# Performance work log

Measured on AMD Instinct MI355X. Metric: run time of the kernel, lower is better.

The kernel has to match this reference:

```python
import jax, jax.numpy as jnp
import numpy as np

M = 50000   # query points
N = 50000   # support points (non-strided: M == N)
C = 128     # channels
H = 32      # neighborhood size
G = 8       # groups
CPG = C // G  # channels per group = 16
R = 1       # alpha_reduction
EPS = 1e-5
NEG_SLOPE = 0.1


def setup_inputs() -> dict:
    key = jax.random.key(0)
    ks = jax.random.split(key, 6)
    q_pts = jax.random.normal(ks[0], (M, 3), jnp.float32)
    s_pts = jax.random.normal(ks[1], (N, 3), jnp.float32)
    s_feats = jax.random.normal(ks[2], (N, C), jnp.float32)
    neighb_inds = jax.random.randint(ks[3], (M, H), 0, N)
    # alpha MLP params: UnaryBlock(C -> C//R) [Linear + BN + LeakyReLU], then Linear(C//R -> H*CPG)
    w1 = jax.random.normal(ks[4], (C, C // R), jnp.float32) * (1.0 / np.sqrt(C))
    b1 = jnp.zeros((C // R,), jnp.float32)
    gamma1 = jnp.ones((C // R,), jnp.float32)
    beta1 = jnp.zeros((C // R,), jnp.float32)
    w2 = jax.random.normal(ks[5], (C // R, H * CPG), jnp.float32) * (1.0 / np.sqrt(C // R))
    b2 = jnp.zeros((H * CPG,), jnp.float32)
    return {"q_pts": q_pts, "s_pts": s_pts, "s_feats": s_feats,
            "neighb_inds": neighb_inds,
            "w1": w1, "b1": b1, "gamma1": gamma1, "beta1": beta1,
            "w2": w2, "b2": b2}


def _alpha_mlp(x, w1, b1, gamma1, beta1, w2, b2):
    # UnaryBlock: Linear -> BatchNorm (training mode over point dim) -> LeakyReLU(0.1)
    h = x @ w1 + b1
    mu = jnp.mean(h, axis=0)
    var = jnp.var(h, axis=0)
    h = (h - mu) * jax.lax.rsqrt(var + EPS) * gamma1 + beta1
    h = jnp.where(h >= 0, h, NEG_SLOPE * h)
    return h @ w2 + b2  # (M, H*CPG)


def reference(q_pts, s_pts, s_feats, neighb_inds, w1, b1, gamma1, beta1, w2, b2):
    # pad support features with a zero "shadow" row so index N maps to zeros
    padded = jnp.concatenate([s_feats, jnp.zeros_like(s_feats[:1])], axis=0)  # (N+1, C)
    neighbor_feats = padded[neighb_inds]  # (M, H, C) gather
    # q_pts.shape[0] == s_pts.shape[0] -> non-strided: pooled feats are the support feats
    pooled_feats = s_feats  # (M, C)
    attn = _alpha_mlp(pooled_feats, w1, b1, gamma1, beta1, w2, b2)  # (M, H*CPG)
    # view: channels dim C splits row-major into (CPG, G)
    nb = neighbor_feats.reshape(M, H, CPG, G)
    a = attn.reshape(M, H, CPG)
    out = jnp.einsum('mhcg,mhc->mcg', nb, a)  # weighted neighbor reduction over H
    return out.reshape(M, C)
```

## Files before the change

### kernel.cpp

```cpp
#include <hip/hip_runtime.h>
#include <hip/hip_bf16.h>

#define MPTS  50000
#define NCH   128
#define NH    32
#define NK2   512
#define NEG   0.1f
#define BN_EPS 1e-5f
#define K1_BLOCKS 1563
#define TPAD_ROWS 50048
#define R1_CHUNK  17
#define R1_BLOCKS 92

typedef __attribute__((ext_vector_type(8))) short        short8;
typedef __attribute__((ext_vector_type(4))) float        float4v;
typedef __attribute__((ext_vector_type(2))) unsigned int uint2v;

__device__ __forceinline__ short f2b(float f) {
    __hip_bfloat16 h = __float2bfloat16(f);
    return *reinterpret_cast<short*>(&h);
}
__device__ __forceinline__ float b2f(short s) {
    unsigned int u = ((unsigned int)(unsigned short)s) << 16;
    return *reinterpret_cast<float*>(&u);
}

__global__ __launch_bounds__(64)
void k0_pack_w1(const float* __restrict__ w1, short* __restrict__ w1f) {
    int o = blockIdx.x * 64 + threadIdx.x;
    int i = o & 7, l = (o >> 3) & 63, ks = (o >> 9) & 3, nt = o >> 11;
    w1f[o] = f2b(w1[(ks * 32 + (l >> 4) * 8 + i) * NCH + nt * 16 + (l & 15)]);
}
__global__ __launch_bounds__(64)
void k0_pack_w2(const float* __restrict__ w2, short* __restrict__ w2f) {
    int o = blockIdx.x * 64 + threadIdx.x;
    int i = o & 7, l = (o >> 3) & 63, ks = (o >> 9) & 3, nt = o >> 11;
    w2f[o] = f2b(w2[(ks * 32 + (l >> 4) * 8 + i) * NK2 + nt * 16 + (l & 15)]);
}

__global__ __launch_bounds__(64)
void k1_gemm(const float* __restrict__ sf, const short* __restrict__ w1f,
             short* __restrict__ t, short* __restrict__ sfb,
             float* __restrict__ pS, float* __restrict__ pSS) {
    const int l = threadIdx.x, lr = l & 15, lg = l >> 4;
    const int m0 = blockIdx.x * 32;

    short8 af[2][4];
    #pragma unroll
    for (int mt = 0; mt < 2; ++mt) {
        const int row = m0 + mt * 16 + lr;
        const bool valid = row < MPTS;
        #pragma unroll
        for (int ks = 0; ks < 4; ++ks) {
            const int col = ks * 32 + lg * 8;
            float4v v0 = {0.f, 0.f, 0.f, 0.f}, v1 = {0.f, 0.f, 0.f, 0.f};
            if (valid) {
                const float4v* p = (const float4v*)(sf + (size_t)row * NCH + col);
                v0 = p[0]; v1 = p[1];
            }
            short8 av;
            av[0] = f2b(v0[0]); av[1] = f2b(v0[1]); av[2] = f2b(v0[2]); av[3] = f2b(v0[3]);
            av[4] = f2b(v1[0]); av[5] = f2b(v1[1]); av[6] = f2b(v1[2]); av[7] = f2b(v1[3]);
            af[mt][ks] = av;
            if (valid) *(short8*)(sfb + (size_t)row * NCH + col) = av;
        }
    }

    float4v acc[2][8];
    #pragma unroll
    for (int mt = 0; mt < 2; ++mt)
        #pragma unroll
        for (int nt = 0; nt < 8; ++nt) acc[mt][nt] = (float4v){0.f, 0.f, 0.f, 0.f};

    #pragma unroll
    for (int nt = 0; nt < 8; ++nt) {
        short8 bq[4];
        #pragma unroll
        for (int ks = 0; ks < 4; ++ks)
            bq[ks] = *(const short8*)(w1f + ((nt * 4 + ks) * 64 + l) * 8);
        #pragma unroll
        for (int ks = 0; ks < 4; ++ks) {
            acc[0][nt] = __builtin_amdgcn_mfma_f32_16x16x32_bf16(af[0][ks], bq[ks], acc[0][nt], 0, 0, 0);
            acc[1][nt] = __builtin_amdgcn_mfma_f32_16x16x32_bf16(af[1][ks], bq[ks], acc[1][nt], 0, 0, 0);
        }
    }

    #pragma unroll
    for (int nt = 0; nt < 8; ++nt) {
        const int cch = nt * 16 + lr;
        float s = 0.f, ss = 0.f;
        #pragma unroll
        for (int mt = 0; mt < 2; ++mt) {
            #pragma unroll
            for (int r = 0; r < 4; ++r) {
                const float v = acc[mt][nt][r];
                const int row = m0 + mt * 16 + lg * 4 + r;
                t[(size_t)row * NCH + cch] = f2b(v);
                s += v; ss += v * v;
            }
        }
        s  += __shfl_xor(s, 16);  s  += __shfl_xor(s, 32);
        ss += __shfl_xor(ss, 16); ss += __shfl_xor(ss, 32);
        if (lg == 0) {
            pS [blockIdx.x * NCH + cch] = s;
            pSS[blockIdx.x * NCH + cch] = ss;
        }
    }
}

__global__ __launch_bounds__(256)
void k2a_reduce(const float* __restrict__ pS, const float* __restrict__ pSS,
                float* __restrict__ qS, float* __restrict__ qSS) {
    const int c = threadIdx.x & 127, a = threadIdx.x >> 7;
    const float* __restrict__ src = a ? pSS : pS;
    const int b0 = blockIdx.x * R1_CHUNK;
    float s = 0.f;
    #pragma unroll
    for (int i = 0; i < R1_CHUNK; ++i) {
        const int b = b0 + i;
        if (b < K1_BLOCKS) s += src[b * NCH + c];
    }
    (a ? qSS : qS)[blockIdx.x * NCH + c] = s;
}

__global__ __launch_bounds__(256)
void k2b_coef(const float* __restrict__ qS, const float* __restrict__ qSS,
              const float* __restrict__ gamma, const float* __restrict__ beta,
              float* __restrict__ coef) {
    __shared__ float sh[256];
    const int c = threadIdx.x & 127, a = threadIdx.x >> 7;
    const float* __restrict__ src = a ? qSS : qS;
    float s0 = 0.f, s1 = 0.f, s2 = 0.f, s3 = 0.f;
    #pragma unroll
    for (int b = 0; b < R1_BLOCKS; b += 4) {
        s0 += src[(b + 0) * NCH + c];
        s1 += src[(b + 1) * NCH + c];
        s2 += src[(b + 2) * NCH + c];
        s3 += src[(b + 3) * NCH + c];
    }
    sh[threadIdx.x] = (s0 + s1) + (s2 + s3);
    __syncthreads();
    if (a == 0) {
        const float inv = 1.0f / (float)MPTS;
        const float mu  = sh[c] * inv;
        const float var = sh[128 + c] * inv - mu * mu;
        const float aa  = gamma[c] * rsqrtf(var + BN_EPS);
        coef[c]       = aa;
        coef[NCH + c] = beta[c] - mu * aa;
    }
}

__global__ __launch_bounds__(256)
void k3_fused(const short* __restrict__ t, const float* __restrict__ coef,
              const short* __restrict__ w2f, const float* __restrict__ b2,
              const short* __restrict__ sfb, const int* __restrict__ nidx,
              float* __restrict__ out) {
    __shared__ short hsh[512 * 8];
    __shared__ short attnT[NK2 * 36];
    __shared__ int   idxs[32 * NH];

    const int tid = threadIdx.x;
    const int m0  = blockIdx.x * 32;

    #pragma unroll
    for (int g = tid; g < 512; g += 256) {
        const int row = g >> 4, ch = g & 15;
        short8 tv = *(const short8*)(t + (size_t)(m0 + row) * NCH + ch * 8);
        const float4v* ca = (const float4v*)(coef + ch * 8);
        const float4v* cb = (const float4v*)(coef + NCH + ch * 8);
        const float4v a0 = ca[0], a1 = ca[1], b0 = cb[0], b1 = cb[1];
        short8 hv;
        #pragma unroll
        for (int j = 0; j < 4; ++j) {
            float x = b2f(tv[j]) * a0[j] + b0[j];
            x = (x >= 0.f) ? x : NEG * x;
            hv[j] = f2b(x);
        }
        #pragma unroll
        for (int j = 0; j < 4; ++j) {
            float x = b2f(tv[4 + j]) * a1[j] + b1[j];
            x = (x >= 0.f) ? x : NEG * x;
            hv[4 + j] = f2b(x);
        }
        *(short8*)&hsh[(row * 16 + (ch ^ (row & 15))) * 8] = hv;
    }
    for (int i2 = tid; i2 < 32 * NH; i2 += 256) {
        const int gi = m0 * NH + i2;
        idxs[i2] = (gi < MPTS * NH) ? nidx[gi] : 0;
    }
    __syncthreads();

    {
        const int l = tid & 63, w = tid >> 6, lr = l & 15, lg = l >> 4;
        short8 af[2][4];
        #pragma unroll
        for (int mt = 0; mt < 2; ++mt)
            #pragma unroll
            for (int ks = 0; ks < 4; ++ks)
                af[mt][ks] = *(const short8*)&hsh[((mt * 16 + lr) * 16 + ((ks * 4 + lg) ^ lr)) * 8];

        #pragma unroll
        for (int nti = 0; nti < 8; ++nti) {
            const int nt = w * 8 + nti;
            float4v acc0 = {0.f, 0.f, 0.f, 0.f}, acc1 = {0.f, 0.f, 0.f, 0.f};
            #pragma unroll
            for (int ks = 0; ks < 4; ++ks) {
                const short8 bq = *(const short8*)(w2f + ((nt * 4 + ks) * 64 + l) * 8);
                acc0 = __builtin_amdgcn_mfma_f32_16x16x32_bf16(af[0][ks], bq, acc0, 0, 0, 0);
                acc1 = __builtin_amdgcn_mfma_f32_16x16x32_bf16(af[1][ks], bq, acc1, 0, 0, 0);
            }
            const int   n    = nt * 16 + lr;
            const float bias = b2[n];
            {
                unsigned u0 = ((unsigned)(unsigned short)f2b(acc0[1] + bias) << 16) |
                               (unsigned short)f2b(acc0[0] + bias);
                unsigned u1 = ((unsigned)(unsigned short)f2b(acc0[3] + bias) << 16) |
                               (unsigned short)f2b(acc0[2] + bias);
                *(uint2v*)&attnT[n * 36 + 0 * 16 + lg * 4] = (uint2v){u0, u1};
            }
            {
                unsigned u0 = ((unsigned)(unsigned short)f2b(acc1[1] + bias) << 16) |
                               (unsigned short)f2b(acc1[0] + bias);
                unsigned u1 = ((unsigned)(unsigned short)f2b(acc1[3] + bias) << 16) |
                               (unsigned short)f2b(acc1[2] + bias);
                *(uint2v*)&attnT[n * 36 + 1 * 16 + lg * 4] = (uint2v){u0, u1};
            }
        }
    }
    __syncthreads();

    {
        const int q = tid & 31, pg = tid >> 5;
        const int c0 = q * 4, cpg = q >> 1;
        #pragma unroll
        for (int pi = 0; pi < 4; ++pi) {
            const int p = pg * 4 + pi, m = m0 + p;
            if (m >= MPTS) continue;
            float4v acc = {0.f, 0.f, 0.f, 0.f};
            #pragma unroll 16
            for (int h = 0; h < NH; ++h) {
                const int n = idxs[p * NH + h];
                const uint2v ld = *(const uint2v*)(sfb + (size_t)n * NCH + c0);
                const float wgt = b2f(attnT[(h * 16 + cpg) * 36 + p]);
                const short* fs = (const short*)&ld;
                acc[0] += b2f(fs[0]) * wgt;
                acc[1] += b2f(fs[1]) * wgt;
                acc[2] += b2f(fs[2]) * wgt;
                acc[3] += b2f(fs[3]) * wgt;
            }
            *(float4v*)(out + (size_t)m * NCH + c0) = acc;
        }
    }
}

extern "C" void kernel_launch(void* const* d_in, const int* in_sizes, int n_in,
                              void* d_out, int out_size, void* d_ws, size_t ws_size,
                              hipStream_t stream) {
    const float* sf    = (const float*)d_in[2];
    const int*   nidx  = (const int*)  d_in[3];
    const float* w1    = (const float*)d_in[4];
    const float* gamma = (const float*)d_in[6];
    const float* beta  = (const float*)d_in[7];
    const float* w2    = (const float*)d_in[8];
    const float* b2    = (const float*)d_in[9];
    float* out = (float*)d_out;

    short* t   = (short*)d_ws;
    short* sfb = t + (size_t)TPAD_ROWS * NCH;
    short* w1f = sfb + (size_t)TPAD_ROWS * NCH;
    short* w2f = w1f + 16384;
    float* pS  = (float*)(w2f + 65536);
    float* pSS = pS + (size_t)K1_BLOCKS * NCH;
    float* qS  = pSS + (size_t)K1_BLOCKS * NCH;
    float* qSS = qS + (size_t)R1_BLOCKS * NCH;
    float* coef = qSS + (size_t)R1_BLOCKS * NCH;

    k0_pack_w1<<<256,  64, 0, stream>>>(w1, w1f);
    k0_pack_w2<<<1024, 64, 0, stream>>>(w2, w2f);
    k1_gemm<<<K1_BLOCKS, 64, 0, stream>>>(sf, w1f, t, sfb, pS, pSS);
    k2a_reduce<<<R1_BLOCKS, 256, 0, stream>>>(pS, pSS, qS, qSS);
    k2b_coef<<<1, 256, 0, stream>>>(qS, qSS, gamma, beta, coef);
    k3_fused<<<K1_BLOCKS, 256, 0, stream>>>(t, coef, w2f, b2, sfb, nidx, out);
}
```

Before: 89.92 us.

## Store GEMM1 output in MFMA fragment layout, halve k3 tile, widen gather loads

k1 now writes the first GEMM result in MFMA accumulator-fragment order as packed 8-byte stores, instead of scattered 2-byte row-major stores. k3 reads those fragments directly for the BN/LeakyReLU prologue. k3 tiles are now 16 points per block, giving twice as many blocks and smaller LDS. The gather stage loads 16 bytes per lane (8 bf16 channels) instead of 8. The two weight-pack kernels are merged into one launch, and k1 runs four waves per block with padded tiles so k2a can drop its bounds checks. The aim is to cut scattered global writes, launch overhead and load instruction count, at the cost of fewer MFMA per block and reliance on padded workspace sizes (k1 tiles past MPTS must produce zero contributions).

```diff
diff --git a/kernel.cpp b/kernel.cpp
--- a/kernel.cpp
+++ b/kernel.cpp
@@ -7,14 +7,17 @@
 #define NK2   512
 #define NEG   0.1f
 #define BN_EPS 1e-5f
-#define K1_BLOCKS 1563
+#define K1T   1564
 #define TPAD_ROWS 50048
 #define R1_CHUNK  17
 #define R1_BLOCKS 92
+#define K3_BLOCKS 3125
+#define ATP 20
 
 typedef __attribute__((ext_vector_type(8))) short        short8;
 typedef __attribute__((ext_vector_type(4))) float        float4v;
 typedef __attribute__((ext_vector_type(2))) unsigned int uint2v;
+typedef __attribute__((ext_vector_type(4))) unsigned int uint4v;
 
 __device__ __forceinline__ short f2b(float f) {
     __hip_bfloat16 h = __float2bfloat16(f);
@@ -24,26 +27,36 @@
     unsigned int u = ((unsigned int)(unsigned short)s) << 16;
     return *reinterpret_cast<float*>(&u);
 }
+__device__ __forceinline__ float b2f_hi(unsigned int w) {
+    unsigned int u = w & 0xffff0000u;
+    return *reinterpret_cast<float*>(&u);
+}
+__device__ __forceinline__ float b2f_lo(unsigned int w) {
+    unsigned int u = w << 16;
+    return *reinterpret_cast<float*>(&u);
+}
 
 __global__ __launch_bounds__(64)
-void k0_pack_w1(const float* __restrict__ w1, short* __restrict__ w1f) {
-    int o = blockIdx.x * 64 + threadIdx.x;
-    int i = o & 7, l = (o >> 3) & 63, ks = (o >> 9) & 3, nt = o >> 11;
-    w1f[o] = f2b(w1[(ks * 32 + (l >> 4) * 8 + i) * NCH + nt * 16 + (l & 15)]);
-}
-__global__ __launch_bounds__(64)
-void k0_pack_w2(const float* __restrict__ w2, short* __restrict__ w2f) {
-    int o = blockIdx.x * 64 + threadIdx.x;
-    int i = o & 7, l = (o >> 3) & 63, ks = (o >> 9) & 3, nt = o >> 11;
-    w2f[o] = f2b(w2[(ks * 32 + (l >> 4) * 8 + i) * NK2 + nt * 16 + (l & 15)]);
-}
-
-__global__ __launch_bounds__(64)
+void k0_pack(const float* __restrict__ w1, const float* __restrict__ w2,
+             short* __restrict__ w1f, short* __restrict__ w2f) {
+    if (blockIdx.x < 256) {
+        int o = blockIdx.x * 64 + threadIdx.x;
+        int i = o & 7, l = (o >> 3) & 63, ks = (o >> 9) & 3, nt = o >> 11;
+        w1f[o] = f2b(w1[(ks * 32 + (l >> 4) * 8 + i) * NCH + nt * 16 + (l & 15)]);
+    } else {
+        int o = (blockIdx.x - 256) * 64 + threadIdx.x;
+        int i = o & 7, l = (o >> 3) & 63, ks = (o >> 9) & 3, nt = o >> 11;
+        w2f[o] = f2b(w2[(ks * 32 + (l >> 4) * 8 + i) * NK2 + nt * 16 + (l & 15)]);
+    }
+}
+
+__global__ __launch_bounds__(256)
 void k1_gemm(const float* __restrict__ sf, const short* __restrict__ w1f,
-             short* __restrict__ t, short* __restrict__ sfb,
+             uint2v* __restrict__ tfrag, short* __restrict__ sfb,
              float* __restrict__ pS, float* __restrict__ pSS) {
-    const int l = threadIdx.x, lr = l & 15, lg = l >> 4;
-    const int m0 = blockIdx.x * 32;
+    const int l = threadIdx.x & 63, lr = l & 15, lg = l >> 4;
+    const int tile = blockIdx.x * 4 + (threadIdx.x >> 6);
+    const int m0 = tile * 32;
 
     short8 af[2][4];
     #pragma unroll
@@ -91,19 +104,18 @@
         float s = 0.f, ss = 0.f;
         #pragma unroll
         for (int mt = 0; mt < 2; ++mt) {
-            #pragma unroll
-            for (int r = 0; r < 4; ++r) {
-                const float v = acc[mt][nt][r];
-                const int row = m0 + mt * 16 + lg * 4 + r;
-                t[(size_t)row * NCH + cch] = f2b(v);
-                s += v; ss += v * v;
-            }
+            const float4v a = acc[mt][nt];
+            unsigned u0 = ((unsigned)(unsigned short)f2b(a[1]) << 16) | (unsigned short)f2b(a[0]);
+            unsigned u1 = ((unsigned)(unsigned short)f2b(a[3]) << 16) | (unsigned short)f2b(a[2]);
+            tfrag[(size_t)((tile * 2 + mt) * 8 + nt) * 64 + l] = (uint2v){u0, u1};
+            s  += a[0] + a[1] + a[2] + a[3];
+            ss += a[0]*a[0] + a[1]*a[1] + a[2]*a[2] + a[3]*a[3];
         }
         s  += __shfl_xor(s, 16);  s  += __shfl_xor(s, 32);
         ss += __shfl_xor(ss, 16); ss += __shfl_xor(ss, 32);
         if (lg == 0) {
-            pS [blockIdx.x * NCH + cch] = s;
-            pSS[blockIdx.x * NCH + cch] = ss;
+            pS [tile * NCH + cch] = s;
+            pSS[tile * NCH + cch] = ss;
         }
     }
 }
@@ -116,10 +128,8 @@
     const int b0 = blockIdx.x * R1_CHUNK;
     float s = 0.f;
     #pragma unroll
-    for (int i = 0; i < R1_CHUNK; ++i) {
-        const int b = b0 + i;
-        if (b < K1_BLOCKS) s += src[b * NCH + c];
-    }
+    for (int i = 0; i < R1_CHUNK; ++i)
+        s += src[(b0 + i) * NCH + c];
     (a ? qSS : qS)[blockIdx.x * NCH + c] = s;
 }
 
@@ -151,105 +161,94 @@
 }
 
 __global__ __launch_bounds__(256)
-void k3_fused(const short* __restrict__ t, const float* __restrict__ coef,
+void k3_fused(const uint2v* __restrict__ tfrag, const float* __restrict__ coef,
               const short* __restrict__ w2f, const float* __restrict__ b2,
               const short* __restrict__ sfb, const int* __restrict__ nidx,
               float* __restrict__ out) {
-    __shared__ short hsh[512 * 8];
-    __shared__ short attnT[NK2 * 36];
-    __shared__ int   idxs[32 * NH];
+    __shared__ short hsh[16 * 128];
+    __shared__ short attnT[NK2 * ATP];
+    __shared__ int   idxs[16 * NH];
 
     const int tid = threadIdx.x;
-    const int m0  = blockIdx.x * 32;
-
-    #pragma unroll
-    for (int g = tid; g < 512; g += 256) {
-        const int row = g >> 4, ch = g & 15;
-        short8 tv = *(const short8*)(t + (size_t)(m0 + row) * NCH + ch * 8);
-        const float4v* ca = (const float4v*)(coef + ch * 8);
-        const float4v* cb = (const float4v*)(coef + NCH + ch * 8);
-        const float4v a0 = ca[0], a1 = ca[1], b0 = cb[0], b1 = cb[1];
-        short8 hv;
-        #pragma unroll
-        for (int j = 0; j < 4; ++j) {
-            float x = b2f(tv[j]) * a0[j] + b0[j];
-            x = (x >= 0.f) ? x : NEG * x;
-            hv[j] = f2b(x);
-        }
-        #pragma unroll
-        for (int j = 0; j < 4; ++j) {
-            float x = b2f(tv[4 + j]) * a1[j] + b1[j];
-            x = (x >= 0.f) ? x : NEG * x;
-            hv[4 + j] = f2b(x);
-        }
-        *(short8*)&hsh[(row * 16 + (ch ^ (row & 15))) * 8] = hv;
-    }
-    for (int i2 = tid; i2 < 32 * NH; i2 += 256) {
-        const int gi = m0 * NH + i2;
-        idxs[i2] = (gi < MPTS * NH) ? nidx[gi] : 0;
+    const int m0  = blockIdx.x * 16;
+
+    {
+        const int l = tid & 63, half = tid >> 6;
+        #pragma unroll
+        for (int k = 0; k < 2; ++k) {
+            const int nt = half + k * 4;
+            const uint2v v = tfrag[(size_t)blockIdx.x * 512 + nt * 64 + l];
+            const int col = nt * 16 + (l & 15);
+            const int rg  = (l >> 4) * 4;
+            const float a = coef[col];
+            const float b = coef[NCH + col];
+            const int ch  = col >> 3;
+            const int cb  = col & 7;
+            float x0 = b2f_lo(v[0]) * a + b;  x0 = (x0 >= 0.f) ? x0 : NEG * x0;
+            float x1 = b2f_hi(v[0]) * a + b;  x1 = (x1 >= 0.f) ? x1 : NEG * x1;
+            float x2 = b2f_lo(v[1]) * a + b;  x2 = (x2 >= 0.f) ? x2 : NEG * x2;
+            float x3 = b2f_hi(v[1]) * a + b;  x3 = (x3 >= 0.f) ? x3 : NEG * x3;
+            hsh[((rg + 0) * 16 + (ch ^ (rg + 0))) * 8 + cb] = f2b(x0);
+            hsh[((rg + 1) * 16 + (ch ^ (rg + 1))) * 8 + cb] = f2b(x1);
+            hsh[((rg + 2) * 16 + (ch ^ (rg + 2))) * 8 + cb] = f2b(x2);
+            hsh[((rg + 3) * 16 + (ch ^ (rg + 3))) * 8 + cb] = f2b(x3);
+        }
+        idxs[tid]       = nidx[(size_t)m0 * NH + tid];
+        idxs[tid + 256] = nidx[(size_t)m0 * NH + tid + 256];
     }
     __syncthreads();
 
     {
         const int l = tid & 63, w = tid >> 6, lr = l & 15, lg = l >> 4;
-        short8 af[2][4];
-        #pragma unroll
-        for (int mt = 0; mt < 2; ++mt)
-            #pragma unroll
-            for (int ks = 0; ks < 4; ++ks)
-                af[mt][ks] = *(const short8*)&hsh[((mt * 16 + lr) * 16 + ((ks * 4 + lg) ^ lr)) * 8];
+        short8 af[4];
+        #pragma unroll
+        for (int ks = 0; ks < 4; ++ks)
+            af[ks] = *(const short8*)&hsh[(lr * 16 + ((ks * 4 + lg) ^ lr)) * 8];
 
         #pragma unroll
         for (int nti = 0; nti < 8; ++nti) {
             const int nt = w * 8 + nti;
-            float4v acc0 = {0.f, 0.f, 0.f, 0.f}, acc1 = {0.f, 0.f, 0.f, 0.f};
+            float4v acc = {0.f, 0.f, 0.f, 0.f};
             #pragma unroll
             for (int ks = 0; ks < 4; ++ks) {
                 const short8 bq = *(const short8*)(w2f + ((nt * 4 + ks) * 64 + l) * 8);
-                acc0 = __builtin_amdgcn_mfma_f32_16x16x32_bf16(af[0][ks], bq, acc0, 0, 0, 0);
-                acc1 = __builtin_amdgcn_mfma_f32_16x16x32_bf16(af[1][ks], bq, acc1, 0, 0, 0);
+                acc = __builtin_amdgcn_mfma_f32_16x16x32_bf16(af[ks], bq, acc, 0, 0, 0);
             }
             const int   n    = nt * 16 + lr;
             const float bias = b2[n];
-            {
-                unsigned u0 = ((unsigned)(unsigned short)f2b(acc0[1] + bias) << 16) |
-                               (unsigned short)f2b(acc0[0] + bias);
-                unsigned u1 = ((unsigned)(unsigned short)f2b(acc0[3] + bias) << 16) |
-                               (unsigned short)f2b(acc0[2] + bias);
-                *(uint2v*)&attnT[n * 36 + 0 * 16 + lg * 4] = (uint2v){u0, u1};
-            }
-            {
-                unsigned u0 = ((unsigned)(unsigned short)f2b(acc1[1] + bias) << 16) |
-                               (unsigned short)f2b(acc1[0] + bias);
-                unsigned u1 = ((unsigned)(unsigned short)f2b(acc1[3] + bias) << 16) |
-                               (unsigned short)f2b(acc1[2] + bias);
-                *(uint2v*)&attnT[n * 36 + 1 * 16 + lg * 4] = (uint2v){u0, u1};
-            }
+            unsigned u0 = ((unsigned)(unsigned short)f2b(acc[1] + bias) << 16) |
+                           (unsigned short)f2b(acc[0] + bias);
+            unsigned u1 = ((unsigned)(unsigned short)f2b(acc[3] + bias) << 16) |
+                           (unsigned short)f2b(acc[2] + bias);
+            *(uint2v*)&attnT[n * ATP + lg * 4] = (uint2v){u0, u1};
         }
     }
     __syncthreads();
 
     {
-        const int q = tid & 31, pg = tid >> 5;
-        const int c0 = q * 4, cpg = q >> 1;
-        #pragma unroll
-        for (int pi = 0; pi < 4; ++pi) {
-            const int p = pg * 4 + pi, m = m0 + p;
-            if (m >= MPTS) continue;
-            float4v acc = {0.f, 0.f, 0.f, 0.f};
-            #pragma unroll 16
-            for (int h = 0; h < NH; ++h) {
-                const int n = idxs[p * NH + h];
-                const uint2v ld = *(const uint2v*)(sfb + (size_t)n * NCH + c0);
-                const float wgt = b2f(attnT[(h * 16 + cpg) * 36 + p]);
-                const short* fs = (const short*)&ld;
-                acc[0] += b2f(fs[0]) * wgt;
-                acc[1] += b2f(fs[1]) * wgt;
-                acc[2] += b2f(fs[2]) * wgt;
-                acc[3] += b2f(fs[3]) * wgt;
-            }
-            *(float4v*)(out + (size_t)m * NCH + c0) = acc;
-        }
+        const int q = tid & 15, p = tid >> 4;
+        const int c0 = q * 8;
+        const int m = m0 + p;
+        float acc0 = 0.f, acc1 = 0.f, acc2 = 0.f, acc3 = 0.f;
+        float acc4 = 0.f, acc5 = 0.f, acc6 = 0.f, acc7 = 0.f;
+        #pragma unroll 4
+        for (int h = 0; h < NH; ++h) {
+            const int n = idxs[p * NH + h];
+            const uint4v ld = *(const uint4v*)(sfb + (size_t)n * NCH + c0);
+            const float wgt = b2f(attnT[(h * 16 + q) * ATP + p]);
+            acc0 += b2f_lo(ld[0]) * wgt;
+            acc1 += b2f_hi(ld[0]) * wgt;
+            acc2 += b2f_lo(ld[1]) * wgt;
+            acc3 += b2f_hi(ld[1]) * wgt;
+            acc4 += b2f_lo(ld[2]) * wgt;
+            acc5 += b2f_hi(ld[2]) * wgt;
+            acc6 += b2f_lo(ld[3]) * wgt;
+            acc7 += b2f_hi(ld[3]) * wgt;
+        }
+        float4v o0 = {acc0, acc1, acc2, acc3};
+        float4v o1 = {acc4, acc5, acc6, acc7};
+        *(float4v*)(out + (size_t)m * NCH + c0)     = o0;
+        *(float4v*)(out + (size_t)m * NCH + c0 + 4) = o1;
     }
 }
 
@@ -265,20 +264,20 @@
     const float* b2    = (const float*)d_in[9];
     float* out = (float*)d_out;
 
-    short* t   = (short*)d_ws;
-    short* sfb = t + (size_t)TPAD_ROWS * NCH;
-    short* w1f = sfb + (size_t)TPAD_ROWS * NCH;
-    short* w2f = w1f + 16384;
-    float* pS  = (float*)(w2f + 65536);
-    float* pSS = pS + (size_t)K1_BLOCKS * NCH;
-    float* qS  = pSS + (size_t)K1_BLOCKS * NCH;
-    float* qSS = qS + (size_t)R1_BLOCKS * NCH;
-    float* coef = qSS + (size_t)R1_BLOCKS * NCH;
-
-    k0_pack_w1<<<256,  64, 0, stream>>>(w1, w1f);
-    k0_pack_w2<<<1024, 64, 0, stream>>>(w2, w2f);
-    k1_gemm<<<K1_BLOCKS, 64, 0, stream>>>(sf, w1f, t, sfb, pS, pSS);
+    short*  t    = (short*)d_ws;
+    short*  sfb  = t + (size_t)TPAD_ROWS * NCH;
+    short*  w1f  = sfb + (size_t)TPAD_ROWS * NCH;
+    short*  w2f  = w1f + 16384;
+    float*  pS   = (float*)(w2f + 65536);
+    float*  pSS  = pS + (size_t)K1T * NCH;
+    float*  qS   = pSS + (size_t)K1T * NCH;
+    float*  qSS  = qS + (size_t)R1_BLOCKS * NCH;
+    float*  coef = qSS + (size_t)R1_BLOCKS * NCH;
+    uint2v* tfrag = (uint2v*)t;
+
+    k0_pack<<<1280, 64, 0, stream>>>(w1, w2, w1f, w2f);
+    k1_gemm<<<391, 256, 0, stream>>>(sf, w1f, tfrag, sfb, pS, pSS);
     k2a_reduce<<<R1_BLOCKS, 256, 0, stream>>>(pS, pSS, qS, qSS);
     k2b_coef<<<1, 256, 0, stream>>>(qS, qSS, gamma, beta, coef);
-    k3_fused<<<K1_BLOCKS, 256, 0, stream>>>(t, coef, w2f, b2, sfb, nidx, out);
-}
+    k3_fused<<<K3_BLOCKS, 256, 0, stream>>>(tfrag, coef, w2f, b2, sfb, nidx, out);
+}
```

Measured after the change: 79.41 us. -11.7%, faster.
